# Kernel optimization log

Hardware: AMD Instinct MI355X
Metric: run time of the kernel (lower is better)

The kernel has to match this reference:

```python
import jax, jax.numpy as jnp
import numpy as np

N_NODES = 100000
N_EDGES = 1600000
IN_FEATURES = 128
OUT_FEATURES = 32


def setup_inputs() -> dict:
    key = jax.random.key(0)
    k_x, k_w, k_r, k_c, k_v = jax.random.split(key, 5)
    x = jax.random.normal(k_x, (N_NODES, IN_FEATURES), dtype=jnp.float32)
    # One fused (in_features, out_features) weight == concat of the out_features Dense(in,1) layers
    W = jax.random.normal(k_w, (IN_FEATURES, OUT_FEATURES), dtype=jnp.float32) / np.sqrt(IN_FEATURES)
    b = jnp.zeros((OUT_FEATURES,), dtype=jnp.float32)
    edge_rows = jax.random.randint(k_r, (N_EDGES,), 0, N_NODES, dtype=jnp.int64)
    edge_cols = jax.random.randint(k_c, (N_EDGES,), 0, N_NODES, dtype=jnp.int64)
    edge_vals = jax.random.uniform(k_v, (N_EDGES,), dtype=jnp.float32)
    return {"x": x, "W": W, "b": b, "edge_rows": edge_rows,
            "edge_cols": edge_cols, "edge_vals": edge_vals}


def reference(x, W, b, edge_rows, edge_cols, edge_vals):
    # z_i = dense_i(x) for all i at once: (N, out_features)
    z = x @ W + b
    # per nonzero edge e=(r,c) with adjacency value w_e:
    #   (z*adj).values + (z^T*adj).values = w_e * (z[r] + z[c])   -> (E, out_features)
    out = edge_vals[:, None] * (z[edge_rows] + z[edge_cols])
    return out
```

## Files before the change

### kernel.cpp

```cpp
#include <hip/hip_runtime.h>

#define NODES 100000
#define IN_F 128
#define OUT_F 32

__global__ __launch_bounds__(256) void zgemm_kernel(
    const float* __restrict__ x, const float* __restrict__ W,
    const float* __restrict__ b, float* __restrict__ z, int n_nodes)
{
    __shared__ float xs[64 * IN_F];
    __shared__ float Ws[IN_F * OUT_F];
    __shared__ float bs[OUT_F];

    const int t = threadIdx.x;
    const int row0 = blockIdx.x * 64;
    const int rows = min(64, n_nodes - row0);

    {
        const float4* Wv = (const float4*)W;
        float4* Wsv = (float4*)Ws;
        #pragma unroll
        for (int i = 0; i < 4; ++i)
            Wsv[t + i * 256] = Wv[t + i * 256];
        if (t < OUT_F) bs[t] = b[t];
    }
    {
        const float4* xv = (const float4*)(x + (size_t)row0 * IN_F);
        float4* xsv = (float4*)xs;
        const int nv = rows * (IN_F / 4);
        for (int i = t; i < nv; i += 256)
            xsv[i] = xv[i];
    }
    __syncthreads();

    const int col = t & 31;
    const int rg  = t >> 5;

    float acc[8];
    #pragma unroll
    for (int i = 0; i < 8; ++i) acc[i] = 0.f;

    for (int k = 0; k < IN_F; ++k) {
        const float wv = Ws[k * OUT_F + col];
        #pragma unroll
        for (int i = 0; i < 8; ++i)
            acc[i] += xs[(rg + i * 8) * IN_F + k] * wv;
    }

    const float bb = bs[col];
    #pragma unroll
    for (int i = 0; i < 8; ++i) {
        const int r = rg + i * 8;
        if (r < rows)
            z[(size_t)(row0 + r) * OUT_F + col] = acc[i] + bb;
    }
}

__global__ __launch_bounds__(256) void edge_kernel(
    const int* __restrict__ erows, const int* __restrict__ ecols,
    const float* __restrict__ evals, const float* __restrict__ z,
    float* __restrict__ out, int n_edges)
{
    const size_t g = (size_t)blockIdx.x * 256 + threadIdx.x;
    const size_t e = g >> 3;
    if (e >= (size_t)n_edges) return;
    const int joff = (int)(g & 7) << 2;

    const int r = erows[e];
    const int c = ecols[e];
    const float w = evals[e];

    const float4 zr = *(const float4*)(z + (size_t)r * OUT_F + joff);
    const float4 zc = *(const float4*)(z + (size_t)c * OUT_F + joff);

    float4 o;
    o.x = w * (zr.x + zc.x);
    o.y = w * (zr.y + zc.y);
    o.z = w * (zr.z + zc.z);
    o.w = w * (zr.w + zc.w);

    *(float4*)(out + e * OUT_F + joff) = o;
}

extern "C" void kernel_launch(void* const* d_in, const int* in_sizes, int n_in,
                              void* d_out, int out_size, void* d_ws, size_t ws_size,
                              hipStream_t stream)
{
    const float* x  = (const float*)d_in[0];
    const float* W  = (const float*)d_in[1];
    const float* b  = (const float*)d_in[2];
    const int* erow = (const int*)d_in[3];
    const int* ecol = (const int*)d_in[4];
    const float* ev = (const float*)d_in[5];

    const int n_nodes = in_sizes[0] / IN_F;
    const int n_edges = in_sizes[3];

    float* z   = (float*)d_ws;
    float* out = (float*)d_out;

    const int gemm_blocks = (n_nodes + 63) / 64;
    zgemm_kernel<<<gemm_blocks, 256, 0, stream>>>(x, W, b, z, n_nodes);

    const size_t total_thr = (size_t)n_edges * 8;
    const int edge_blocks = (int)((total_thr + 255) / 256);
    edge_kernel<<<edge_blocks, 256, 0, stream>>>(erow, ecol, ev, z, out, n_edges);
}
```

Baseline: 326.8 us.

## Transpose W in LDS, vectorize GEMM reads, nontemporal edge I/O, grid-stride edges

The GEMM now stores W transposed with padding in shared memory and reads x and W as 4-wide vectors, cutting the number of LDS loads in the inner loop. The x tile is loaded with nontemporal hints. The edge kernel uses a grid-stride loop capped at 4096 blocks, with nontemporal loads of the edge arrays and nontemporal stores of the large output, to reduce cache pollution and launch overhead. Risks include LDS bank conflicts from the vector reads of x and less latency hiding with the capped grid.

```diff
diff --git a/kernel.cpp b/kernel.cpp
--- a/kernel.cpp
+++ b/kernel.cpp
@@ -1,15 +1,17 @@
 #include <hip/hip_runtime.h>
 
-#define NODES 100000
 #define IN_F 128
 #define OUT_F 32
+#define WT_LD 132
+
+typedef float vf4 __attribute__((ext_vector_type(4)));
 
 __global__ __launch_bounds__(256) void zgemm_kernel(
     const float* __restrict__ x, const float* __restrict__ W,
     const float* __restrict__ b, float* __restrict__ z, int n_nodes)
 {
     __shared__ float xs[64 * IN_F];
-    __shared__ float Ws[IN_F * OUT_F];
+    __shared__ float Wt[OUT_F * WT_LD];
     __shared__ float bs[OUT_F];
 
     const int t = threadIdx.x;
@@ -17,19 +19,26 @@
     const int rows = min(64, n_nodes - row0);
 
     {
-        const float4* Wv = (const float4*)W;
-        float4* Wsv = (float4*)Ws;
+        const vf4* Wv = (const vf4*)W;
         #pragma unroll
-        for (int i = 0; i < 4; ++i)
-            Wsv[t + i * 256] = Wv[t + i * 256];
+        for (int i = 0; i < 4; ++i) {
+            const int idx4 = t + i * 256;
+            const vf4 w = Wv[idx4];
+            const int k  = idx4 >> 3;
+            const int c0 = (idx4 & 7) << 2;
+            Wt[(c0 + 0) * WT_LD + k] = w.x;
+            Wt[(c0 + 1) * WT_LD + k] = w.y;
+            Wt[(c0 + 2) * WT_LD + k] = w.z;
+            Wt[(c0 + 3) * WT_LD + k] = w.w;
+        }
         if (t < OUT_F) bs[t] = b[t];
     }
     {
-        const float4* xv = (const float4*)(x + (size_t)row0 * IN_F);
-        float4* xsv = (float4*)xs;
+        const vf4* xv = (const vf4*)(x + (size_t)row0 * IN_F);
+        vf4* xsv = (vf4*)xs;
         const int nv = rows * (IN_F / 4);
         for (int i = t; i < nv; i += 256)
-            xsv[i] = xv[i];
+            xsv[i] = __builtin_nontemporal_load(xv + i);
     }
     __syncthreads();
 
@@ -40,11 +49,18 @@
     #pragma unroll
     for (int i = 0; i < 8; ++i) acc[i] = 0.f;
 
-    for (int k = 0; k < IN_F; ++k) {
-        const float wv = Ws[k * OUT_F + col];
+    const vf4* Wc = (const vf4*)(Wt + col * WT_LD);
+    #pragma unroll 4
+    for (int k4 = 0; k4 < IN_F / 4; ++k4) {
+        const vf4 w4 = Wc[k4];
         #pragma unroll
-        for (int i = 0; i < 8; ++i)
-            acc[i] += xs[(rg + i * 8) * IN_F + k] * wv;
+        for (int i = 0; i < 8; ++i) {
+            const vf4 x4 = *(const vf4*)(xs + (rg + i * 8) * IN_F + (k4 << 2));
+            acc[i] += x4.x * w4.x;
+            acc[i] += x4.y * w4.y;
+            acc[i] += x4.z * w4.z;
+            acc[i] += x4.w * w4.w;
+        }
     }
 
     const float bb = bs[col];
@@ -61,25 +77,27 @@
     const float* __restrict__ evals, const float* __restrict__ z,
     float* __restrict__ out, int n_edges)
 {
-    const size_t g = (size_t)blockIdx.x * 256 + threadIdx.x;
-    const size_t e = g >> 3;
-    if (e >= (size_t)n_edges) return;
-    const int joff = (int)(g & 7) << 2;
+    const size_t total  = (size_t)n_edges * 8;
+    const size_t stride = (size_t)gridDim.x * 256;
+    for (size_t g = (size_t)blockIdx.x * 256 + threadIdx.x; g < total; g += stride) {
+        const size_t e = g >> 3;
+        const int joff = (int)(g & 7) << 2;
 
-    const int r = erows[e];
-    const int c = ecols[e];
-    const float w = evals[e];
+        const int   r = __builtin_nontemporal_load(erows + e);
+        const int   c = __builtin_nontemporal_load(ecols + e);
+        const float w = __builtin_nontemporal_load(evals + e);
 
-    const float4 zr = *(const float4*)(z + (size_t)r * OUT_F + joff);
-    const float4 zc = *(const float4*)(z + (size_t)c * OUT_F + joff);
+        const vf4 zr = *(const vf4*)(z + (size_t)r * OUT_F + joff);
+        const vf4 zc = *(const vf4*)(z + (size_t)c * OUT_F + joff);
 
-    float4 o;
-    o.x = w * (zr.x + zc.x);
-    o.y = w * (zr.y + zc.y);
-    o.z = w * (zr.z + zc.z);
-    o.w = w * (zr.w + zc.w);
+        vf4 o;
+        o.x = w * (zr.x + zc.x);
+        o.y = w * (zr.y + zc.y);
+        o.z = w * (zr.z + zc.z);
+        o.w = w * (zr.w + zc.w);
 
-    *(float4*)(out + e * OUT_F + joff) = o;
+        __builtin_nontemporal_store(o, (vf4*)(out + e * OUT_F + joff));
+    }
 }
 
 extern "C" void kernel_launch(void* const* d_in, const int* in_sizes, int n_in,
@@ -103,6 +121,7 @@
     zgemm_kernel<<<gemm_blocks, 256, 0, stream>>>(x, W, b, z, n_nodes);
 
     const size_t total_thr = (size_t)n_edges * 8;
-    const int edge_blocks = (int)((total_thr + 255) / 256);
+    int edge_blocks = (int)((total_thr + 255) / 256);
+    if (edge_blocks > 4096) edge_blocks = 4096;
     edge_kernel<<<edge_blocks, 256, 0, stream>>>(erow, ecol, ev, z, out, n_edges);
 }
```

New measurement: 341.1 us. 4.4% more time.
